# Optimization experiments

Measured on AMD Instinct MI355X. Metric: run time of the kernel, lower is better.

The kernel has to match this reference:

```python
import jax, jax.numpy as jnp
import numpy as np

W_REG = 3.0
N_CAND = 4
IOU_LEN = 15.0
BIG_COST = 1e8


def focal_cost(cls_pred, gt_labels, alpha=0.25, gamma=2.0, eps=1e-12):
    # cls_pred: [B,P,C] logits, gt_labels: [B,T] int -> [B,P,T]
    p = jax.nn.sigmoid(cls_pred)
    neg = -jnp.log(1.0 - p + eps) * (1.0 - alpha) * p ** gamma
    pos = -jnp.log(p + eps) * alpha * (1.0 - p) ** gamma
    B, P, _ = cls_pred.shape
    T = gt_labels.shape[1]
    idx = jnp.broadcast_to(gt_labels[:, None, :], (B, P, T))
    return jnp.take_along_axis(pos, idx, axis=2) - jnp.take_along_axis(neg, idx, axis=2)


def line_iou(pred, target, img_w, length=IOU_LEN):
    # pred: [B,P,O], target: [B,T,O] -> [B,P,T] (unaligned)
    px1, px2 = pred - length, pred + length
    tx1, tx2 = target - length, target + length
    ovr = jnp.minimum(px2[:, :, None, :], tx2[:, None, :, :]) - jnp.maximum(px1[:, :, None, :], tx1[:, None, :, :])
    union = jnp.maximum(px2[:, :, None, :], tx2[:, None, :, :]) - jnp.minimum(px1[:, :, None, :], tx1[:, None, :, :])
    invalid = ((target < 0) | (target >= img_w))[:, None, :, :]
    ovr = jnp.where(invalid, 0.0, ovr)
    union = jnp.where(invalid, 0.0, union)
    return ovr.sum(-1) / (union.sum(-1) + 1e-9)


def clrnet_assign(preds, targets, masks, img_w, img_h):
    B, P, _ = preds.shape
    T = targets.shape[1]
    w = float(img_w - 1)
    h = float(img_h - 1)
    pa = preds.at[..., 3].multiply(w).at[..., 6:].multiply(w)
    ta = targets.at[..., 3].multiply(w).at[..., 6:].multiply(w)
    p_off, t_off = pa[..., 6:], ta[..., 6:]

    # --- distance score (masked mean L1 over valid target x-offsets) ---
    tvalid = (t_off >= 0) & (t_off < img_w)                      # [B,T,O]
    cmask = tvalid[:, None, :, :]                                 # [B,1,T,O]
    clen = jnp.maximum(cmask.sum(-1).astype(pa.dtype), 1.0)      # [B,1,T]
    diff = jnp.abs(p_off[:, :, None, :] - t_off[:, None, :, :]) * cmask  # [B,P,T,O]
    distances = diff.sum(-1) / clen                               # [B,P,T]
    dist_max = jnp.maximum(distances.max(axis=(1, 2), keepdims=True), 1e-8)
    dist_score = 1.0 - distances / dist_max + 0.01

    # --- start-point score (euclidean on (y*(h), x)) ---
    ps = pa[..., 2:4].at[..., 0].multiply(h)
    ts = ta[..., 2:4].at[..., 0].multiply(h)
    start_d = jnp.sqrt(((ps[:, :, None, :] - ts[:, None, :, :]) ** 2).sum(-1))
    start_max = jnp.maximum(start_d.max(axis=(1, 2), keepdims=True), 1e-8)
    start_score = 1.0 - start_d / start_max + 0.01

    # --- theta score ---
    th_d = jnp.abs(pa[..., 4][:, :, None] - ta[..., 4][:, None, :]) * 180.0
    th_max = jnp.maximum(th_d.max(axis=(1, 2), keepdims=True), 1e-8)
    th_score = 1.0 - th_d / th_max + 0.01

    # --- total cost ---
    gt_labels = ta[..., 1].astype(jnp.int32)
    cls_cost = focal_cost(pa[..., :2], gt_labels)
    reg = (jnp.maximum(dist_score, 1e-3) * jnp.maximum(start_score, 1e-3)
           * jnp.maximum(th_score, 1e-3))
    total_cost = -(reg ** 2) * W_REG + cls_cost                   # [B,P,T]
    valid_t = (masks > 0)[:, None, :]                             # [B,1,T]
    total_cost = jnp.where(valid_t, total_cost, BIG_COST)

    # --- dynamic-k from line IoU ---
    liou = jnp.nan_to_num(line_iou(p_off, t_off, img_w), nan=0.0)
    liou = jnp.where(valid_t, liou, 0.0)
    k = min(N_CAND, P)
    topk_ious, _ = jax.lax.top_k(jnp.swapaxes(liou, 1, 2), k)     # [B,T,k]
    dynamic_ks = jnp.maximum(topk_ious.sum(-1).astype(jnp.int32), 1)
    dynamic_ks = jnp.where(masks > 0, dynamic_ks, 0)              # [B,T]

    # --- top-k lowest-cost priors per target, scatter into matching matrix ---
    _, topk_idx = jax.lax.top_k(-jnp.swapaxes(total_cost, 1, 2), k)  # [B,T,k]
    sel = (jnp.arange(k)[None, None, :] < dynamic_ks[:, :, None]).astype(total_cost.dtype)  # [B,T,k]
    one_hot_p = jax.nn.one_hot(topk_idx, P, dtype=total_cost.dtype)  # [B,T,k,P]
    matching = jnp.swapaxes((one_hot_p * sel[..., None]).sum(2), 1, 2)  # [B,P,T]

    # --- conflict resolution: a prior matched to >1 targets keeps argmin-cost one ---
    conflict = matching.sum(-1) > 1                               # [B,P]
    masked_cost = jnp.where(matching == 0, jnp.inf, total_cost)
    best_t = jnp.argmin(masked_cost, axis=2)                      # [B,P]
    new_m = jax.nn.one_hot(best_t, T, dtype=matching.dtype)
    matching = jnp.where(conflict[..., None], new_m, matching)

    has_match = matching.sum(-1) > 0.5
    t_idx = jnp.argmax(matching, axis=2)
    matched = jnp.where(has_match, t_idx, -1).astype(jnp.int32)
    return matched >= 0, matched


def setup_inputs() -> dict:
    key = jax.random.key(0)
    k1, k2, k3 = jax.random.split(key, 3)
    B, P, T, O = 32, 1000, 16, 72
    D = 6 + O
    preds = jax.random.uniform(k1, (B, P, D), dtype=jnp.float32)
    # slightly outside [0,1] so the invalid-offset masking path is exercised
    targets = jax.random.uniform(k2, (B, T, D), dtype=jnp.float32, minval=-0.05, maxval=1.05)
    masks = jax.random.randint(k3, (B, T), 0, 2).astype(jnp.int32)
    return {"preds": preds, "targets": targets, "masks": masks, "img_w": 800, "img_h": 320}


def reference(preds, targets, masks, img_w, img_h):
    return clrnet_assign(preds, targets, masks, img_w, img_h)
```

## Files before the change

kernel.cpp:

```cpp
#include <hip/hip_runtime.h>
#include <math.h>

#define B_ 32
#define P_ 1000
#define T_ 16
#define D_ 78
#define O_ 72
#define NXB 16
#define BIGC 100000000.0f

__global__ __launch_bounds__(1024, 8) void k1(
        const float* __restrict__ preds, const float* __restrict__ targets,
        const int* __restrict__ imgw_p, const int* __restrict__ imgh_p,
        float* __restrict__ dist, float* __restrict__ liou,
        float4* __restrict__ scal4, float* __restrict__ pths,
        float* __restrict__ pmax) {
    __shared__ float pred_s[64 * 81];
    __shared__ float2 tomg[T_ * O_];
    __shared__ float Spart[T_][4][64];
    __shared__ float wmax[16][3];
    __shared__ float cnt_s[T_], clen_s[T_], ts0_s[T_], ts1_s[T_], tth_s[T_];

    const int b = blockIdx.y, bx = blockIdx.x;
    const int p0 = bx * 64;
    const int rows = min(64, P_ - p0);
    const int tid = threadIdx.x;
    const float w = (float)(imgw_p[0] - 1);
    const float h = (float)(imgh_p[0] - 1);
    const float imgwf = (float)imgw_p[0];

    {
        const float4* gbase = (const float4*)(preds + ((size_t)b * P_ + p0) * D_);
        const int n4 = rows * D_ / 4;
        for (int i = tid; i < n4; i += 1024) {
            float4 v = gbase[i];
            int base = i * 4;
            int r = base / D_, c = base - r * D_;
#pragma unroll
            for (int k = 0; k < 4; ++k) {
                int cc = c + k, rr = r;
                if (cc >= D_) { cc -= D_; ++rr; }
                float x = (&v.x)[k];
                if (cc >= 6 || cc == 3) x *= w;
                pred_s[rr * 81 + cc] = x;
            }
        }
    }
    for (int i = tid; i < T_ * O_; i += 1024) {
        int t = i / O_, o = i - t * O_;
        float to = targets[((size_t)b * T_ + t) * D_ + 6 + o] * w;
        float m = (to >= 0.f && to < imgwf) ? 1.f : 0.f;
        tomg[((t >> 2) * O_ + o) * 4 + (t & 3)] = make_float2(to, m);
    }
    __syncthreads();
    if (tid < T_) {
        int t = tid;
        float c = 0.f;
        for (int o = 0; o < O_; ++o) c += tomg[((t >> 2) * O_ + o) * 4 + (t & 3)].y;
        cnt_s[t] = c;
        clen_s[t] = fmaxf(c, 1.f);
        const float* tr = targets + ((size_t)b * T_ + t) * D_;
        ts0_s[t] = tr[2] * h;
        ts1_s[t] = tr[3] * w;
        tth_s[t] = tr[4];
    }
    __syncthreads();

    {
        const int lane = tid & 63;
        const int wv = tid >> 6;
        const int tg = wv & 3;
        const int oq = wv >> 2;
        const float* lrow = pred_s + lane * 81;
        const float4* tg4 = (const float4*)(tomg + (size_t)tg * O_ * 4);
        const int o_lo = oq * 18;
        float S0 = 0.f, S1 = 0.f, S2 = 0.f, S3 = 0.f;
#pragma unroll
        for (int i = 0; i < 18; ++i) {
            int o = o_lo + i;
            float po = lrow[6 + o];
            float4 r0 = tg4[2 * o];
            float4 r1 = tg4[2 * o + 1];
            S0 += r0.y * fabsf(po - r0.x);
            S1 += r0.w * fabsf(po - r0.z);
            S2 += r1.y * fabsf(po - r1.x);
            S3 += r1.w * fabsf(po - r1.z);
        }
        Spart[4 * tg + 0][oq][lane] = S0;
        Spart[4 * tg + 1][oq][lane] = S1;
        Spart[4 * tg + 2][oq][lane] = S2;
        Spart[4 * tg + 3][oq][lane] = S3;
    }
    __syncthreads();

    const int th = tid >> 6, pl = tid & 63;
    const int p = p0 + pl;
    float ldm = 0.f, lsm = 0.f, ltm = 0.f;
    if (pl < rows) {
        float S = ((Spart[th][0][pl] + Spart[th][1][pl]) + Spart[th][2][pl]) + Spart[th][3][pl];
        float dv = S / clen_s[th];
        dist[(size_t)(b * T_ + th) * P_ + p] = dv;
        ldm = dv;
        float c30 = 30.f * cnt_s[th];
        liou[(size_t)(b * T_ + th) * P_ + p] = (c30 - S) / (c30 + S + 1e-9f);
        const float* prow = pred_s + pl * 81;
        float ps0 = prow[2] * h, ps1 = prow[3], pth = prow[4];
        float d0 = ps0 - ts0_s[th], d1 = ps1 - ts1_s[th];
        lsm = sqrtf(d0 * d0 + d1 * d1);
        ltm = fabsf(pth - tth_s[th]) * 180.f;
        if (th == 0) {
            float fc[2];
#pragma unroll
            for (int c = 0; c < 2; ++c) {
                float x = prow[c];
                float pc = 1.f / (1.f + expf(-x));
                float neg = -logf(1.f - pc + 1e-12f) * 0.75f * pc * pc;
                float pos = -logf(pc + 1e-12f) * 0.25f * (1.f - pc) * (1.f - pc);
                fc[c] = pos - neg;
            }
            scal4[(size_t)b * P_ + p] = make_float4(fc[0], fc[1], ps0, ps1);
            pths[(size_t)b * P_ + p] = pth;
        }
    }

    for (int off = 32; off; off >>= 1) {
        ldm = fmaxf(ldm, __shfl_xor(ldm, off, 64));
        lsm = fmaxf(lsm, __shfl_xor(lsm, off, 64));
        ltm = fmaxf(ltm, __shfl_xor(ltm, off, 64));
    }
    if (pl == 0) { wmax[th][0] = ldm; wmax[th][1] = lsm; wmax[th][2] = ltm; }
    __syncthreads();
    if (tid == 0) {
        float m0 = 0.f, m1 = 0.f, m2 = 0.f;
#pragma unroll
        for (int i = 0; i < 16; ++i) {
            m0 = fmaxf(m0, wmax[i][0]);
            m1 = fmaxf(m1, wmax[i][1]);
            m2 = fmaxf(m2, wmax[i][2]);
        }
        float* q = pmax + (size_t)(b * NXB + bx) * 3;
        q[0] = m0; q[1] = m1; q[2] = m2;
    }
}

__global__ __launch_bounds__(1024) void k2(
        const float* __restrict__ targets, const int* __restrict__ masks,
        const int* __restrict__ imgw_p, const int* __restrict__ imgh_p,
        const float* __restrict__ dist, const float* __restrict__ liou,
        const float4* __restrict__ scal4, const float* __restrict__ pths,
        const float* __restrict__ pmax,
        float* __restrict__ cost, int* __restrict__ out) {
    __shared__ int selE[64];

    const int b = blockIdx.x;
    const int tid = threadIdx.x;
    const int t = tid >> 6;
    const int lane = tid & 63;

    float dm = 0.f, sm = 0.f, tm = 0.f;
    for (int i = 0; i < NXB; ++i) {
        const float* q = pmax + (size_t)(b * NXB + i) * 3;
        dm = fmaxf(dm, q[0]); sm = fmaxf(sm, q[1]); tm = fmaxf(tm, q[2]);
    }
    dm = fmaxf(dm, 1e-8f); sm = fmaxf(sm, 1e-8f); tm = fmaxf(tm, 1e-8f);

    const float w = (float)(imgw_p[0] - 1);
    const float h = (float)(imgh_p[0] - 1);
    const float* tr = targets + (size_t)(b * T_ + t) * D_;
    const float ts0 = tr[2] * h, ts1 = tr[3] * w, tth = tr[4];
    int lab = (int)tr[1]; lab = lab < 0 ? 0 : (lab > 1 ? 1 : lab);
    const int mk = masks[b * T_ + t];

    const float* drow = dist + (size_t)(b * T_ + t) * P_;
    const float* lrow = liou + (size_t)(b * T_ + t) * P_;
    float* crow = cost + (size_t)(b * T_ + t) * P_;
    const float4* s4b = scal4 + (size_t)b * P_;
    const float* ptb = pths + (size_t)b * P_;

    float lv[16], cv[16];
#pragma unroll
    for (int i = 0; i < 16; ++i) {
        int p = lane + 64 * i;
        if (p < P_) {
            float d = drow[p];
            float4 s4 = s4b[p];
            float pth = ptb[p];
            float dsc = 1.f - d / dm + 0.01f;
            float d0 = s4.z - ts0, d1 = s4.w - ts1;
            float ssc = 1.f - sqrtf(d0 * d0 + d1 * d1) / sm + 0.01f;
            float tsc = 1.f - fabsf(pth - tth) * 180.f / tm + 0.01f;
            float reg = fmaxf(dsc, 1e-3f) * fmaxf(ssc, 1e-3f) * fmaxf(tsc, 1e-3f);
            float c = -(reg * reg) * 3.f + (lab ? s4.y : s4.x);
            if (mk <= 0) c = BIGC;
            crow[p] = c;
            cv[i] = c;
            lv[i] = lrow[p];
        } else {
            cv[i] = INFINITY;
            lv[i] = -INFINITY;
        }
    }

    float sum = 0.f;
    for (int r = 0; r < 4; ++r) {
        float bv = -INFINITY; int bi = 0x7fffffff;
#pragma unroll
        for (int i = 0; i < 16; ++i) {
            if (lv[i] > bv) { bv = lv[i]; bi = lane + 64 * i; }
        }
        for (int off = 32; off; off >>= 1) {
            float ov = __shfl_xor(bv, off, 64);
            int oi = __shfl_xor(bi, off, 64);
            if (ov > bv || (ov == bv && oi < bi)) { bv = ov; bi = oi; }
        }
        sum += bv;
        if ((bi & 63) == lane) lv[bi >> 6] = -INFINITY;
    }
    int dk = 0;
    if (mk > 0) {
        dk = (int)sum;
        if (dk < 1) dk = 1;
        if (dk > 4) dk = 4;
    }

    int selp[4];
#pragma unroll
    for (int r = 0; r < 4; ++r) {
        float bv = INFINITY; int bi = 0x7fffffff;
#pragma unroll
        for (int i = 0; i < 16; ++i) {
            if (cv[i] < bv) { bv = cv[i]; bi = lane + 64 * i; }
        }
        for (int off = 32; off; off >>= 1) {
            float ov = __shfl_xor(bv, off, 64);
            int oi = __shfl_xor(bi, off, 64);
            if (ov < bv || (ov == bv && oi < bi)) { bv = ov; bi = oi; }
        }
        selp[r] = bi;
        if ((bi & 63) == lane) cv[bi >> 6] = INFINITY;
    }

    if (lane == 0) {
#pragma unroll
        for (int j = 0; j < 4; ++j) selE[4 * t + j] = (j < dk) ? selp[j] : -1;
    }
    __syncthreads();

    if (tid < P_) {
        const int p = tid;
        unsigned int m = 0;
#pragma unroll
        for (int t2 = 0; t2 < T_; ++t2) {
            bool hit = (selE[4 * t2] == p) | (selE[4 * t2 + 1] == p) |
                       (selE[4 * t2 + 2] == p) | (selE[4 * t2 + 3] == p);
            if (hit) m |= 1u << t2;
        }
        int matched = -1;
        if (m) {
            if (__popc(m) == 1) {
                matched = __ffs(m) - 1;
            } else {
                float best = INFINITY;
#pragma unroll
                for (int t2 = 0; t2 < T_; ++t2) {
                    if ((m >> t2) & 1u) {
                        float c = cost[(size_t)(b * T_ + t2) * P_ + p];
                        if (c < best) { best = c; matched = t2; }
                    }
                }
            }
        }
        out[b * P_ + p] = (matched >= 0) ? 1 : 0;
        out[B_ * P_ + b * P_ + p] = matched;
    }
}

extern "C" void kernel_launch(void* const* d_in, const int* in_sizes, int n_in,
                              void* d_out, int out_size, void* d_ws, size_t ws_size,
                              hipStream_t stream) {
    const float* preds   = (const float*)d_in[0];
    const float* targets = (const float*)d_in[1];
    const int*   masks   = (const int*)d_in[2];
    const int*   imgw    = (const int*)d_in[3];
    const int*   imgh    = (const int*)d_in[4];
    int* out = (int*)d_out;

    char* ws = (char*)d_ws;
    const size_t SZ = (size_t)B_ * T_ * P_ * sizeof(float);
    float*  dist  = (float*)ws;
    float*  liou  = (float*)(ws + SZ);
    float*  cost  = (float*)(ws + 2 * SZ);
    float4* scal4 = (float4*)(ws + 3 * SZ);
    float*  pths  = (float*)(ws + 3 * SZ + (size_t)B_ * P_ * 16);
    float*  pmax  = (float*)(ws + 3 * SZ + (size_t)B_ * P_ * 20);

    k1<<<dim3(NXB, B_), 1024, 0, stream>>>(preds, targets, imgw, imgh, dist, liou, scal4, pths, pmax);
    k2<<<B_, 1024, 0, stream>>>(targets, masks, imgw, imgh, dist, liou, scal4, pths, pmax, cost, out);
}
```

Measured before the change: 37.60 us.

## Split top-k selection into per-(batch,target) wavefront blocks and separate resolve kernel

The second kernel used 32 blocks of 1024 threads, one per batch. Now it launches 512 single-wavefront blocks, one per (batch, target), so more CUs are busy. Registers are held as unrolled scalars with a deactivation bitmask instead of indexed arrays, which avoids scratch spills. Conflict resolution moves into a new third kernel that reads the selections from workspace, at the cost of one extra launch and a global round-trip.

```diff
diff --git a/kernel.cpp b/kernel.cpp
--- a/kernel.cpp
+++ b/kernel.cpp
@@ -143,19 +143,19 @@
     }
 }
 
-__global__ __launch_bounds__(1024) void k2(
+#define FOREACH16(M) M(0) M(1) M(2) M(3) M(4) M(5) M(6) M(7) \
+                     M(8) M(9) M(10) M(11) M(12) M(13) M(14) M(15)
+
+__global__ __launch_bounds__(64) void k2(
         const float* __restrict__ targets, const int* __restrict__ masks,
         const int* __restrict__ imgw_p, const int* __restrict__ imgh_p,
         const float* __restrict__ dist, const float* __restrict__ liou,
         const float4* __restrict__ scal4, const float* __restrict__ pths,
         const float* __restrict__ pmax,
-        float* __restrict__ cost, int* __restrict__ out) {
-    __shared__ int selE[64];
-
-    const int b = blockIdx.x;
-    const int tid = threadIdx.x;
-    const int t = tid >> 6;
-    const int lane = tid & 63;
+        float* __restrict__ cost, int4* __restrict__ sel) {
+    const int wid = blockIdx.x;
+    const int b = wid >> 4, t = wid & 15;
+    const int lane = threadIdx.x;
 
     float dm = 0.f, sm = 0.f, tm = 0.f;
     for (int i = 0; i < NXB; ++i) {
@@ -177,45 +177,59 @@
     const float4* s4b = scal4 + (size_t)b * P_;
     const float* ptb = pths + (size_t)b * P_;
 
-    float lv[16], cv[16];
-#pragma unroll
-    for (int i = 0; i < 16; ++i) {
-        int p = lane + 64 * i;
-        if (p < P_) {
-            float d = drow[p];
-            float4 s4 = s4b[p];
-            float pth = ptb[p];
-            float dsc = 1.f - d / dm + 0.01f;
-            float d0 = s4.z - ts0, d1 = s4.w - ts1;
-            float ssc = 1.f - sqrtf(d0 * d0 + d1 * d1) / sm + 0.01f;
-            float tsc = 1.f - fabsf(pth - tth) * 180.f / tm + 0.01f;
-            float reg = fmaxf(dsc, 1e-3f) * fmaxf(ssc, 1e-3f) * fmaxf(tsc, 1e-3f);
-            float c = -(reg * reg) * 3.f + (lab ? s4.y : s4.x);
-            if (mk <= 0) c = BIGC;
-            crow[p] = c;
-            cv[i] = c;
-            lv[i] = lrow[p];
-        } else {
-            cv[i] = INFINITY;
-            lv[i] = -INFINITY;
-        }
-    }
+#define DECL(i) float L##i, C##i;
+    FOREACH16(DECL)
+#undef DECL
+
+#define CHUNK(i) {                                                        \
+        int p = lane + 64 * (i);                                          \
+        if (p < P_) {                                                     \
+            float d = drow[p];                                            \
+            float4 s4 = s4b[p];                                           \
+            float pth = ptb[p];                                           \
+            float dsc = 1.f - d / dm + 0.01f;                             \
+            float d0 = s4.z - ts0, d1 = s4.w - ts1;                       \
+            float ssc = 1.f - sqrtf(d0 * d0 + d1 * d1) / sm + 0.01f;      \
+            float tsc = 1.f - fabsf(pth - tth) * 180.f / tm + 0.01f;      \
+            float reg = fmaxf(dsc, 1e-3f) * fmaxf(ssc, 1e-3f) * fmaxf(tsc, 1e-3f); \
+            float c = -(reg * reg) * 3.f + (lab ? s4.y : s4.x);           \
+            if (mk <= 0) c = BIGC;                                        \
+            crow[p] = c;                                                  \
+            C##i = c;                                                     \
+            L##i = lrow[p];                                               \
+        } else {                                                          \
+            C##i = INFINITY;                                              \
+            L##i = -INFINITY;                                             \
+        } }
+    FOREACH16(CHUNK)
+#undef CHUNK
+
+    unsigned int deact;
+    float bv; int bi;
+
+#define SCANMAX(i) { float v = (deact & (1u << (i))) ? -INFINITY : L##i;  \
+        int ix = lane + 64 * (i);                                         \
+        if (v > bv || (v == bv && ix < bi)) { bv = v; bi = ix; } }
+#define SCANMIN(i) { float v = (deact & (1u << (i))) ? INFINITY : C##i;   \
+        int ix = lane + 64 * (i);                                         \
+        if (v < bv || (v == bv && ix < bi)) { bv = v; bi = ix; } }
+#define BFLYMAX for (int off = 32; off; off >>= 1) {                      \
+        float ov = __shfl_xor(bv, off, 64);                               \
+        int oi = __shfl_xor(bi, off, 64);                                 \
+        if (ov > bv || (ov == bv && oi < bi)) { bv = ov; bi = oi; } }
+#define BFLYMIN for (int off = 32; off; off >>= 1) {                      \
+        float ov = __shfl_xor(bv, off, 64);                               \
+        int oi = __shfl_xor(bi, off, 64);                                 \
+        if (ov < bv || (ov == bv && oi < bi)) { bv = ov; bi = oi; } }
+#define DEACT if ((bi & 63) == lane) deact |= 1u << (bi >> 6);
 
     float sum = 0.f;
-    for (int r = 0; r < 4; ++r) {
-        float bv = -INFINITY; int bi = 0x7fffffff;
-#pragma unroll
-        for (int i = 0; i < 16; ++i) {
-            if (lv[i] > bv) { bv = lv[i]; bi = lane + 64 * i; }
-        }
-        for (int off = 32; off; off >>= 1) {
-            float ov = __shfl_xor(bv, off, 64);
-            int oi = __shfl_xor(bi, off, 64);
-            if (ov > bv || (ov == bv && oi < bi)) { bv = ov; bi = oi; }
-        }
-        sum += bv;
-        if ((bi & 63) == lane) lv[bi >> 6] = -INFINITY;
-    }
+    deact = 0;
+#define ROUNDMAX { bv = -INFINITY; bi = 0x7fffffff;                       \
+        FOREACH16(SCANMAX) BFLYMAX sum += bv; DEACT }
+    ROUNDMAX ROUNDMAX ROUNDMAX ROUNDMAX
+#undef ROUNDMAX
+
     int dk = 0;
     if (mk > 0) {
         dk = (int)sum;
@@ -223,37 +237,40 @@
         if (dk > 4) dk = 4;
     }
 
-    int selp[4];
-#pragma unroll
-    for (int r = 0; r < 4; ++r) {
-        float bv = INFINITY; int bi = 0x7fffffff;
-#pragma unroll
-        for (int i = 0; i < 16; ++i) {
-            if (cv[i] < bv) { bv = cv[i]; bi = lane + 64 * i; }
-        }
-        for (int off = 32; off; off >>= 1) {
-            float ov = __shfl_xor(bv, off, 64);
-            int oi = __shfl_xor(bi, off, 64);
-            if (ov < bv || (ov == bv && oi < bi)) { bv = ov; bi = oi; }
-        }
-        selp[r] = bi;
-        if ((bi & 63) == lane) cv[bi >> 6] = INFINITY;
-    }
+    int s0, s1, s2, s3;
+    deact = 0;
+#define ROUNDMIN(sr) { bv = INFINITY; bi = 0x7fffffff;                    \
+        FOREACH16(SCANMIN) BFLYMIN sr = bi; DEACT }
+    ROUNDMIN(s0) ROUNDMIN(s1) ROUNDMIN(s2) ROUNDMIN(s3)
+#undef ROUNDMIN
 
     if (lane == 0) {
-#pragma unroll
-        for (int j = 0; j < 4; ++j) selE[4 * t + j] = (j < dk) ? selp[j] : -1;
-    }
-    __syncthreads();
-
-    if (tid < P_) {
-        const int p = tid;
+        sel[wid] = make_int4(dk > 0 ? s0 : -1, dk > 1 ? s1 : -1,
+                             dk > 2 ? s2 : -1, dk > 3 ? s3 : -1);
+    }
+#undef SCANMAX
+#undef SCANMIN
+#undef BFLYMAX
+#undef BFLYMIN
+#undef DEACT
+}
+
+__global__ __launch_bounds__(256) void k3(const int4* __restrict__ sel,
+                                          const float* __restrict__ cost,
+                                          int* __restrict__ out) {
+    __shared__ int selE[64];
+    const int b = blockIdx.y, cx = blockIdx.x;
+    if (threadIdx.x < 64) selE[threadIdx.x] = ((const int*)sel)[b * 64 + threadIdx.x];
+    __syncthreads();
+
+    const int p = cx * 250 + threadIdx.x;
+    if (threadIdx.x < 250) {
         unsigned int m = 0;
 #pragma unroll
-        for (int t2 = 0; t2 < T_; ++t2) {
-            bool hit = (selE[4 * t2] == p) | (selE[4 * t2 + 1] == p) |
-                       (selE[4 * t2 + 2] == p) | (selE[4 * t2 + 3] == p);
-            if (hit) m |= 1u << t2;
+        for (int t = 0; t < T_; ++t) {
+            bool hit = (selE[4 * t] == p) | (selE[4 * t + 1] == p) |
+                       (selE[4 * t + 2] == p) | (selE[4 * t + 3] == p);
+            if (hit) m |= 1u << t;
         }
         int matched = -1;
         if (m) {
@@ -262,10 +279,10 @@
             } else {
                 float best = INFINITY;
 #pragma unroll
-                for (int t2 = 0; t2 < T_; ++t2) {
-                    if ((m >> t2) & 1u) {
-                        float c = cost[(size_t)(b * T_ + t2) * P_ + p];
-                        if (c < best) { best = c; matched = t2; }
+                for (int t = 0; t < T_; ++t) {
+                    if ((m >> t) & 1u) {
+                        float c = cost[(size_t)(b * T_ + t) * P_ + p];
+                        if (c < best) { best = c; matched = t; }
                     }
                 }
             }
@@ -293,7 +310,9 @@
     float4* scal4 = (float4*)(ws + 3 * SZ);
     float*  pths  = (float*)(ws + 3 * SZ + (size_t)B_ * P_ * 16);
     float*  pmax  = (float*)(ws + 3 * SZ + (size_t)B_ * P_ * 20);
+    int4*   sel   = (int4*)(ws + 3 * SZ + (size_t)B_ * P_ * 20 + (size_t)B_ * NXB * 3 * 4 + 64);
 
     k1<<<dim3(NXB, B_), 1024, 0, stream>>>(preds, targets, imgw, imgh, dist, liou, scal4, pths, pmax);
-    k2<<<B_, 1024, 0, stream>>>(targets, masks, imgw, imgh, dist, liou, scal4, pths, pmax, cost, out);
+    k2<<<B_ * T_, 64, 0, stream>>>(targets, masks, imgw, imgh, dist, liou, scal4, pths, pmax, cost, sel);
+    k3<<<dim3(4, B_), 256, 0, stream>>>(sel, cost, out);
 }
```

Measured after the change: 38.71 us. 1.03x slower.
